# Kernel optimization log

Hardware: AMD Instinct MI355X
Metric: run time of the kernel (lower is better)

The kernel has to match this reference:

```python
import jax, jax.numpy as jnp
import numpy as np

B, N, NC, T, C, H = 8, 16, 16, 64, 512, 8


def setup_inputs() -> dict:
    key = jax.random.key(0)
    ks = jax.random.split(key, 7)
    s = 1.0 / np.sqrt(C)  # ~kaiming-uniform scale for Linear weights
    x = jax.random.normal(ks[0], (B, N, T, C), dtype=jnp.float32)
    c = jax.random.normal(ks[1], (B, NC, T, C), dtype=jnp.float32)
    mask = jax.random.randint(ks[2], (B, N * T, (N + NC) * T), 0, 2).astype(bool)
    Wq = jax.random.normal(ks[3], (C, C), dtype=jnp.float32) * s  # [out, in], torch Linear layout
    Wk = jax.random.normal(ks[4], (C, C), dtype=jnp.float32) * s
    Wv = jax.random.normal(ks[5], (C, C), dtype=jnp.float32) * s
    Wp = jax.random.normal(ks[6], (C, C), dtype=jnp.float32) * s
    return {"x": x, "c": c, "mask": mask, "Wq": Wq, "Wk": Wk, "Wv": Wv, "Wp": Wp}


def reference(x, c, mask, Wq, Wk, Wv, Wp):
    Bx, Nx, Tx, Cx = x.shape
    Dh = Cx // H
    kv_in = jnp.concatenate([x, c], axis=1)           # hybrid: [B, N+NC, T, C]
    Nk = kv_in.shape[1]
    # torch Linear: y = x @ W.T  -> einsum '...c,dc->...d'
    q = jnp.einsum('bntc,dc->bntd', x, Wq).reshape(Bx, Nx * Tx, H, Dh).transpose(0, 2, 1, 3)
    k = jnp.einsum('bntc,dc->bntd', kv_in, Wk).reshape(Bx, Nk * Tx, H, Dh).transpose(0, 2, 1, 3)
    v = jnp.einsum('bntc,dc->bntd', kv_in, Wv).reshape(Bx, Nk * Tx, H, Dh).transpose(0, 2, 1, 3)
    att = jnp.einsum('bhqd,bhkd->bhqk', q, k) * (1.0 / np.sqrt(Dh))  # [B,H,NT,NkT]
    att = jnp.where(mask[:, None, :, :], -jnp.inf, att)
    att = jax.nn.softmax(att, axis=-1)
    y = jnp.einsum('bhqk,bhkd->bhqd', att, v)          # [B,H,NT,Dh]
    y = y.transpose(0, 2, 1, 3).reshape(Bx, Nx * Tx, Cx)
    y = jnp.einsum('btc,dc->btd', y, Wp)
    return y.reshape(Bx, Nx, Tx, Cx)
```

## Files before the change

kernel.cpp:

```cpp
#include <hip/hip_runtime.h>
#include <hip/hip_bf16.h>
#include <stdint.h>

typedef __bf16 v8bf __attribute__((ext_vector_type(8)));
typedef short v4s __attribute__((ext_vector_type(4)));
typedef float f32x4 __attribute__((ext_vector_type(4)));

__device__ __forceinline__ void gload_lds16(const void* g, void* l) {
    __builtin_amdgcn_global_load_lds(
        (const __attribute__((address_space(1))) void*)g,
        (__attribute__((address_space(3))) void*)l, 16, 0, 0);
}

__device__ __forceinline__ unsigned short f2bf(float f) {
    __hip_bfloat16 h = __float2bfloat16(f);
    return __builtin_bit_cast(unsigned short, h);
}

__device__ __forceinline__ f32x4 mfma16x16x16bf(v4s a, v4s b, f32x4 c) {
#if __has_builtin(__builtin_amdgcn_mfma_f32_16x16x16bf16_1k)
    return __builtin_amdgcn_mfma_f32_16x16x16bf16_1k(a, b, c, 0, 0, 0);
#elif __has_builtin(__builtin_amdgcn_mfma_f32_16x16x16_bf16)
    return __builtin_amdgcn_mfma_f32_16x16x16_bf16(a, b, c, 0, 0, 0);
#else
    asm("s_nop 1\n\t"
        "v_mfma_f32_16x16x16_bf16 %0, %1, %2, %0\n\t"
        "s_nop 7\n\ts_nop 3"
        : "+v"(c) : "v"(a), "v"(b));
    return c;
#endif
}

__global__ __launch_bounds__(256) void cvt_xcw(const float* __restrict__ x,
                                               const float* __restrict__ c,
                                               const float* __restrict__ wq,
                                               const float* __restrict__ wk,
                                               const float* __restrict__ wv,
                                               const float* __restrict__ wp,
                                               __hip_bfloat16* __restrict__ xc,
                                               __hip_bfloat16* __restrict__ wout) {
    int bid = blockIdx.x;
    if (bid < 8192) {
        int i = bid * 256 + threadIdx.x;
        long e = (long)i * 4;
        int b = (int)(e >> 20);
        int rem = (int)(e & ((1 << 20) - 1));
        int r = rem >> 9;
        int col = rem & 511;
        const float* src = (r < 1024) ? (x + ((long)b << 19) + (long)r * 512 + col)
                                      : (c + ((long)b << 19) + (long)(r - 1024) * 512 + col);
        float4 v = *(const float4*)src;
        ushort4 o;
        o.x = f2bf(v.x); o.y = f2bf(v.y); o.z = f2bf(v.z); o.w = f2bf(v.w);
        ((ushort4*)xc)[i] = o;
    } else {
        int i = (bid - 8192) * 256 + threadIdx.x;
        int e = i * 4;
        int w = e >> 18;
        int off = e & ((1 << 18) - 1);
        const float* src = (w == 0 ? wq : w == 1 ? wk : w == 2 ? wv : wp) + off;
        float4 val = *(const float4*)src;
        ushort4 o;
        o.x = f2bf(val.x); o.y = f2bf(val.y); o.z = f2bf(val.z); o.w = f2bf(val.w);
        ((ushort4*)wout)[i] = o;
    }
}

__global__ __launch_bounds__(256) void cvt_mask(const int* __restrict__ mask,
                                                unsigned long long* __restrict__ mbt) {
    int t = threadIdx.x;
    long base = (long)blockIdx.x * 1024;
#pragma unroll
    for (int j = 0; j < 4; j++) {
        long i = base + j * 256 + t;
        int v = mask[i] != 0;
        unsigned long long bits = __ballot(v);
        if ((t & 63) == 0) {
            int b = (int)(i >> 21);
            int q = (int)((i >> 11) & 1023);
            int word = (int)((i >> 6) & 31);
            mbt[((long)b * 32 + word) * 1024 + q] = bits;
        }
    }
}

__global__ __launch_bounds__(256) void gemm_qkv(const __hip_bfloat16* __restrict__ A,
                                                const __hip_bfloat16* __restrict__ Bw,
                                                __hip_bfloat16* __restrict__ Qw,
                                                __hip_bfloat16* __restrict__ Kw,
                                                __hip_bfloat16* __restrict__ Vtw) {
    __shared__ union {
        struct { __hip_bfloat16 As[128 * 32]; __hip_bfloat16 Bs[128 * 32]; } s;
        __hip_bfloat16 T[128 * 136];
    } u;
    const int tid = threadIdx.x;
    const int wave = tid >> 6, lane = tid & 63;
    const int m0 = blockIdx.x * 128, n0 = blockIdx.y * 128;

    const int la = lane >> 2;
    const int kc = (lane & 3) * 8;
    const long ga0 = (long)(m0 + wave * 16 + la) * 512 + kc;
    const long ga1 = (long)(m0 + (wave + 4) * 16 + la) * 512 + kc;
    const long gb0 = (long)(n0 + wave * 16 + la) * 512 + kc;
    const long gb1 = (long)(n0 + (wave + 4) * 16 + la) * 512 + kc;

    f32x4 acc[4][4] = {};
    const int mw = (wave & 1) * 64, nw = (wave >> 1) * 64;
    const int lrow = lane & 15, lk = (lane >> 4) * 8;

    for (int k0 = 0; k0 < 512; k0 += 32) {
        gload_lds16(A + ga0 + k0, &u.s.As[wave * 512]);
        gload_lds16(A + ga1 + k0, &u.s.As[(wave + 4) * 512]);
        gload_lds16(Bw + gb0 + k0, &u.s.Bs[wave * 512]);
        gload_lds16(Bw + gb1 + k0, &u.s.Bs[(wave + 4) * 512]);
        __syncthreads();
        v8bf a[4], b[4];
#pragma unroll
        for (int i = 0; i < 4; i++) {
            a[i] = *(const v8bf*)&u.s.As[(mw + i * 16 + lrow) * 32 + lk];
            b[i] = *(const v8bf*)&u.s.Bs[(nw + i * 16 + lrow) * 32 + lk];
        }
#pragma unroll
        for (int mi = 0; mi < 4; mi++)
#pragma unroll
            for (int ni = 0; ni < 4; ni++)
                acc[mi][ni] = __builtin_amdgcn_mfma_f32_16x16x32_bf16(a[mi], b[ni], acc[mi][ni], 0, 0, 0);
        __syncthreads();
    }

    const int lq = lane >> 4;
    if (blockIdx.y < 8) {
#pragma unroll
        for (int mi = 0; mi < 4; mi++)
#pragma unroll
            for (int ni = 0; ni < 4; ni++)
#pragma unroll
                for (int r = 0; r < 4; r++) {
                    int grow = m0 + mw + mi * 16 + lq * 4 + r;
                    int gcol = n0 + nw + ni * 16 + lrow;
                    int w = gcol >> 9, g9 = gcol & 511;
                    int h = g9 >> 6, dh = g9 & 63;
                    int b_ = grow >> 11, rr = grow & 2047;
                    float val = acc[mi][ni][r];
                    if (w == 0) {
                        if (rr < 1024)
                            Qw[((long)(b_ * 8 + h) * 1024 + rr) * 64 + dh] =
                                __float2bfloat16(val * 0.1803368801f);
                    } else {
                        Kw[((long)(b_ * 8 + h) * 2048 + rr) * 64 + dh] = __float2bfloat16(val);
                    }
                }
    } else {
#pragma unroll
        for (int mi = 0; mi < 4; mi++)
#pragma unroll
            for (int ni = 0; ni < 4; ni++) {
                int n_l = nw + ni * 16 + lrow;
                int m_l = mw + mi * 16 + lq * 4;
                ushort4 pk;
                pk.x = f2bf(acc[mi][ni][0]); pk.y = f2bf(acc[mi][ni][1]);
                pk.z = f2bf(acc[mi][ni][2]); pk.w = f2bf(acc[mi][ni][3]);
                *(ushort4*)&u.T[n_l * 136 + m_l] = pk;
            }
        __syncthreads();
        const int no = (blockIdx.y - 8) * 128;
        const int b_ = m0 >> 11, rrb = m0 & 2047;
#pragma unroll
        for (int i = 0; i < 8; i++) {
            int s = tid + i * 256;
            int n_l = s >> 4, ch = s & 15;
            int ng = no + n_l;
            int h = ng >> 6, dh = ng & 63;
            uint4 v = *(const uint4*)&u.T[n_l * 136 + ch * 8];
            *(uint4*)&Vtw[((long)(b_ * 8 + h) * 64 + dh) * 2048 + rrb + ch * 8] = v;
        }
    }
}

__global__ __launch_bounds__(256) void gemm_out(const __hip_bfloat16* __restrict__ A,
                                                const __hip_bfloat16* __restrict__ Bw,
                                                float* __restrict__ outp) {
    __shared__ __hip_bfloat16 As[128 * 32];
    __shared__ __hip_bfloat16 Bs[128 * 32];
    const int tid = threadIdx.x;
    const int wave = tid >> 6, lane = tid & 63;
    const int m0 = blockIdx.x * 128, n0 = blockIdx.y * 128;

    const int la = lane >> 2;
    const int kc = (lane & 3) * 8;
    const long ga0 = (long)(m0 + wave * 16 + la) * 512 + kc;
    const long ga1 = (long)(m0 + (wave + 4) * 16 + la) * 512 + kc;
    const long gb0 = (long)(n0 + wave * 16 + la) * 512 + kc;
    const long gb1 = (long)(n0 + (wave + 4) * 16 + la) * 512 + kc;

    f32x4 acc[4][4] = {};
    const int mw = (wave & 1) * 64, nw = (wave >> 1) * 64;
    const int lrow = lane & 15, lk = (lane >> 4) * 8;

    for (int k0 = 0; k0 < 512; k0 += 32) {
        gload_lds16(A + ga0 + k0, &As[wave * 512]);
        gload_lds16(A + ga1 + k0, &As[(wave + 4) * 512]);
        gload_lds16(Bw + gb0 + k0, &Bs[wave * 512]);
        gload_lds16(Bw + gb1 + k0, &Bs[(wave + 4) * 512]);
        __syncthreads();
        v8bf a[4], b[4];
#pragma unroll
        for (int i = 0; i < 4; i++) {
            a[i] = *(const v8bf*)&As[(mw + i * 16 + lrow) * 32 + lk];
            b[i] = *(const v8bf*)&Bs[(nw + i * 16 + lrow) * 32 + lk];
        }
#pragma unroll
        for (int mi = 0; mi < 4; mi++)
#pragma unroll
            for (int ni = 0; ni < 4; ni++)
                acc[mi][ni] = __builtin_amdgcn_mfma_f32_16x16x32_bf16(a[mi], b[ni], acc[mi][ni], 0, 0, 0);
        __syncthreads();
    }

    const int lq = lane >> 4;
#pragma unroll
    for (int mi = 0; mi < 4; mi++)
#pragma unroll
        for (int ni = 0; ni < 4; ni++)
#pragma unroll
            for (int r = 0; r < 4; r++) {
                int grow = m0 + mw + mi * 16 + lq * 4 + r;
                int gcol = n0 + nw + ni * 16 + lrow;
                outp[(long)grow * 512 + gcol] = acc[mi][ni][r];
            }
}

__global__ __launch_bounds__(256) void flash(const __hip_bfloat16* __restrict__ Q,
                                             const __hip_bfloat16* __restrict__ K,
                                             const __hip_bfloat16* __restrict__ Vt,
                                             const unsigned long long* __restrict__ Mbt,
                                             __hip_bfloat16* __restrict__ Y) {
    constexpr int LDT = 72;
    __shared__ __hip_bfloat16 Ks[2][64 * LDT];
    __shared__ __hip_bfloat16 Vts[2][64 * LDT];

    const int L = blockIdx.x;
    const int b = L & 7, qt = (L >> 3) & 15, h = L >> 7;
    const int bh = b * 8 + h;
    const int tid = threadIdx.x, w = tid >> 6, lane = tid & 63;
    const int lcol = lane & 15, lq = lane >> 4;

    const __hip_bfloat16* Qp = Q + ((long)bh * 1024 + qt * 64 + w * 16 + lcol) * 64 + lq * 8;
    const __hip_bfloat16* Kg = K + (long)bh * 2048 * 64;
    const __hip_bfloat16* Vg = Vt + (long)bh * 64 * 2048;
    const unsigned long long* Mp = Mbt + (long)b * 32 * 1024 + qt * 64 + w * 16 + lcol;

    const int u0 = tid, u1 = tid + 256;
    const int r0 = u0 >> 3, p0 = u0 & 7;
    const int r1 = u1 >> 3, p1 = u1 & 7;

    v8bf bq0 = *(const v8bf*)(Qp);
    v8bf bq1 = *(const v8bf*)(Qp + 32);

    f32x4 O[4] = {};
    float lsum = 0.f;

    {
        const uint4* ksrc = (const uint4*)Kg;
        uint4 k0 = ksrc[u0], k1 = ksrc[u1];
        uint4 v0 = *(const uint4*)(Vg + (long)r0 * 2048 + p0 * 8);
        uint4 v1 = *(const uint4*)(Vg + (long)r1 * 2048 + p1 * 8);
        *(uint4*)&Ks[0][r0 * LDT + p0 * 8] = k0;
        *(uint4*)&Ks[0][r1 * LDT + p1 * 8] = k1;
        *(uint4*)&Vts[0][r0 * LDT + p0 * 8] = v0;
        *(uint4*)&Vts[0][r1 * LDT + p1 * 8] = v1;
    }
    __syncthreads();

    int cur = 0;
    for (int kt = 0; kt < 32; kt++) {
        unsigned long long mword = Mp[(long)kt * 1024];

        uint4 nk0, nk1, nv0, nv1;
        if (kt < 31) {
            const uint4* ksrc = (const uint4*)(Kg + ((kt + 1) << 12));
            nk0 = ksrc[u0];
            nk1 = ksrc[u1];
            nv0 = *(const uint4*)(Vg + (long)r0 * 2048 + (kt + 1) * 64 + p0 * 8);
            nv1 = *(const uint4*)(Vg + (long)r1 * 2048 + (kt + 1) * 64 + p1 * 8);
        }

        const __hip_bfloat16* Kb = Ks[cur];
        const __hip_bfloat16* Vb = Vts[cur];
#pragma unroll
        for (int nt = 0; nt < 4; nt++) {
            v8bf ak0 = *(const v8bf*)&Kb[(nt * 16 + lcol) * LDT + lq * 8];
            v8bf ak1 = *(const v8bf*)&Kb[(nt * 16 + lcol) * LDT + 32 + lq * 8];
            f32x4 st = {};
            __builtin_amdgcn_s_setprio(1);
            st = __builtin_amdgcn_mfma_f32_16x16x32_bf16(ak0, bq0, st, 0, 0, 0);
            st = __builtin_amdgcn_mfma_f32_16x16x32_bf16(ak1, bq1, st, 0, 0, 0);
            __builtin_amdgcn_s_setprio(0);
            unsigned int nib = (unsigned int)(mword >> (nt * 16 + lq * 4)) & 0xFu;
            float e0 = ((nib >> 0) & 1u) ? 0.f : __builtin_amdgcn_exp2f(fminf(st[0], 57.f));
            float e1 = ((nib >> 1) & 1u) ? 0.f : __builtin_amdgcn_exp2f(fminf(st[1], 57.f));
            float e2 = ((nib >> 2) & 1u) ? 0.f : __builtin_amdgcn_exp2f(fminf(st[2], 57.f));
            float e3 = ((nib >> 3) & 1u) ? 0.f : __builtin_amdgcn_exp2f(fminf(st[3], 57.f));
            lsum += (e0 + e1) + (e2 + e3);
            __hip_bfloat162 lo = __float22bfloat162_rn(make_float2(e0, e1));
            __hip_bfloat162 hi = __float22bfloat162_rn(make_float2(e2, e3));
            uint2 pku;
            __builtin_memcpy(&pku.x, &lo, 4);
            __builtin_memcpy(&pku.y, &hi, 4);
            v4s pa = __builtin_bit_cast(v4s, pku);
            __builtin_amdgcn_s_setprio(1);
#pragma unroll
            for (int nd = 0; nd < 4; nd++) {
                v4s bv = *(const v4s*)&Vb[(nd * 16 + lcol) * LDT + nt * 16 + lq * 4];
                O[nd] = mfma16x16x16bf(pa, bv, O[nd]);
            }
            __builtin_amdgcn_s_setprio(0);
        }

        if (kt < 31) {
            __hip_bfloat16* Kw_ = Ks[cur ^ 1];
            __hip_bfloat16* Vw_ = Vts[cur ^ 1];
            *(uint4*)&Kw_[r0 * LDT + p0 * 8] = nk0;
            *(uint4*)&Kw_[r1 * LDT + p1 * 8] = nk1;
            *(uint4*)&Vw_[r0 * LDT + p0 * 8] = nv0;
            *(uint4*)&Vw_[r1 * LDT + p1 * 8] = nv1;
        }
        __syncthreads();
        cur ^= 1;
    }

    float s = lsum;
    s += __shfl_xor(s, 16);
    s += __shfl_xor(s, 32);
    float inv[4];
#pragma unroll
    for (int r = 0; r < 4; r++) inv[r] = 1.f / __shfl(s, lq * 4 + r);

    __hip_bfloat16* Yp = Y + ((long)b * 1024 + qt * 64 + w * 16) * 512 + h * 64 + lcol;
#pragma unroll
    for (int nd = 0; nd < 4; nd++)
#pragma unroll
        for (int r = 0; r < 4; r++)
            Yp[(long)(lq * 4 + r) * 512 + nd * 16] = __float2bfloat16(O[nd][r] * inv[r]);
}

extern "C" void kernel_launch(void* const* d_in, const int* in_sizes, int n_in,
                              void* d_out, int out_size, void* d_ws, size_t ws_size,
                              hipStream_t stream) {
    const float* x = (const float*)d_in[0];
    const float* c = (const float*)d_in[1];
    const int* mask = (const int*)d_in[2];
    const float* Wq = (const float*)d_in[3];
    const float* Wk = (const float*)d_in[4];
    const float* Wv = (const float*)d_in[5];
    const float* Wp = (const float*)d_in[6];

    char* ws = (char*)d_ws;
    __hip_bfloat16* xc  = (__hip_bfloat16*)(ws);
    __hip_bfloat16* Wbf = (__hip_bfloat16*)(ws + 16777216);
    __hip_bfloat16* Qw  = (__hip_bfloat16*)(ws + 18874368);
    __hip_bfloat16* Kw  = (__hip_bfloat16*)(ws + 27262976);
    __hip_bfloat16* Vtw = (__hip_bfloat16*)(ws + 44040192);
    __hip_bfloat16* Yb  = (__hip_bfloat16*)(ws + 60817408);
    unsigned long long* Mbp = (unsigned long long*)(ws);

    cvt_xcw<<<9216, 256, 0, stream>>>(x, c, Wq, Wk, Wv, Wp, xc, Wbf);
    gemm_qkv<<<dim3(128, 12), 256, 0, stream>>>(xc, Wbf, Qw, Kw, Vtw);
    cvt_mask<<<16384, 256, 0, stream>>>(mask, Mbp);
    flash<<<1024, 256, 0, stream>>>(Qw, Kw, Vtw, Mbp, Yb);
    gemm_out<<<dim3(64, 4), 256, 0, stream>>>(Yb, Wbf + 3 * 262144, (float*)d_out);
}
```

Baseline: 281.0 us.

## Double-buffer LDS tiles in QKV/out GEMMs and prefetch mask word in flash

```diff
diff --git a/kernel.cpp b/kernel.cpp
--- a/kernel.cpp
+++ b/kernel.cpp
@@ -90,8 +90,8 @@
                                                 __hip_bfloat16* __restrict__ Kw,
                                                 __hip_bfloat16* __restrict__ Vtw) {
     __shared__ union {
-        struct { __hip_bfloat16 As[128 * 32]; __hip_bfloat16 Bs[128 * 32]; } s;
-        __hip_bfloat16 T[128 * 136];
+        struct { __hip_bfloat16 As[2][128 * 32]; __hip_bfloat16 Bs[2][128 * 32]; } s;
+        __hip_bfloat16 T[64 * 136];
     } u;
     const int tid = threadIdx.x;
     const int wave = tid >> 6, lane = tid & 63;
@@ -108,23 +108,34 @@
     const int mw = (wave & 1) * 64, nw = (wave >> 1) * 64;
     const int lrow = lane & 15, lk = (lane >> 4) * 8;
 
-    for (int k0 = 0; k0 < 512; k0 += 32) {
-        gload_lds16(A + ga0 + k0, &u.s.As[wave * 512]);
-        gload_lds16(A + ga1 + k0, &u.s.As[(wave + 4) * 512]);
-        gload_lds16(Bw + gb0 + k0, &u.s.Bs[wave * 512]);
-        gload_lds16(Bw + gb1 + k0, &u.s.Bs[(wave + 4) * 512]);
-        __syncthreads();
+    gload_lds16(A + ga0, &u.s.As[0][wave * 512]);
+    gload_lds16(A + ga1, &u.s.As[0][(wave + 4) * 512]);
+    gload_lds16(Bw + gb0, &u.s.Bs[0][wave * 512]);
+    gload_lds16(Bw + gb1, &u.s.Bs[0][(wave + 4) * 512]);
+    __syncthreads();
+
+    for (int it = 0; it < 16; ++it) {
+        const int cur = it & 1;
+        if (it < 15) {
+            const int k0 = (it + 1) * 32;
+            gload_lds16(A + ga0 + k0, &u.s.As[cur ^ 1][wave * 512]);
+            gload_lds16(A + ga1 + k0, &u.s.As[cur ^ 1][(wave + 4) * 512]);
+            gload_lds16(Bw + gb0 + k0, &u.s.Bs[cur ^ 1][wave * 512]);
+            gload_lds16(Bw + gb1 + k0, &u.s.Bs[cur ^ 1][(wave + 4) * 512]);
+        }
         v8bf a[4], b[4];
 #pragma unroll
         for (int i = 0; i < 4; i++) {
-            a[i] = *(const v8bf*)&u.s.As[(mw + i * 16 + lrow) * 32 + lk];
-            b[i] = *(const v8bf*)&u.s.Bs[(nw + i * 16 + lrow) * 32 + lk];
-        }
+            a[i] = *(const v8bf*)&u.s.As[cur][(mw + i * 16 + lrow) * 32 + lk];
+            b[i] = *(const v8bf*)&u.s.Bs[cur][(nw + i * 16 + lrow) * 32 + lk];
+        }
+        __builtin_amdgcn_s_setprio(1);
 #pragma unroll
         for (int mi = 0; mi < 4; mi++)
 #pragma unroll
             for (int ni = 0; ni < 4; ni++)
                 acc[mi][ni] = __builtin_amdgcn_mfma_f32_16x16x32_bf16(a[mi], b[ni], acc[mi][ni], 0, 0, 0);
+        __builtin_amdgcn_s_setprio(0);
         __syncthreads();
     }
 
@@ -151,28 +162,34 @@
                     }
                 }
     } else {
-#pragma unroll
-        for (int mi = 0; mi < 4; mi++)
-#pragma unroll
-            for (int ni = 0; ni < 4; ni++) {
-                int n_l = nw + ni * 16 + lrow;
-                int m_l = mw + mi * 16 + lq * 4;
-                ushort4 pk;
-                pk.x = f2bf(acc[mi][ni][0]); pk.y = f2bf(acc[mi][ni][1]);
-                pk.z = f2bf(acc[mi][ni][2]); pk.w = f2bf(acc[mi][ni][3]);
-                *(ushort4*)&u.T[n_l * 136 + m_l] = pk;
-            }
-        __syncthreads();
         const int no = (blockIdx.y - 8) * 128;
         const int b_ = m0 >> 11, rrb = m0 & 2047;
 #pragma unroll
-        for (int i = 0; i < 8; i++) {
-            int s = tid + i * 256;
-            int n_l = s >> 4, ch = s & 15;
-            int ng = no + n_l;
-            int h = ng >> 6, dh = ng & 63;
-            uint4 v = *(const uint4*)&u.T[n_l * 136 + ch * 8];
-            *(uint4*)&Vtw[((long)(b_ * 8 + h) * 64 + dh) * 2048 + rrb + ch * 8] = v;
+        for (int pass = 0; pass < 2; ++pass) {
+            __syncthreads();
+            if ((wave >> 1) == pass) {
+#pragma unroll
+                for (int mi = 0; mi < 4; mi++)
+#pragma unroll
+                    for (int ni = 0; ni < 4; ni++) {
+                        int n_l = ni * 16 + lrow;
+                        int m_l = mw + mi * 16 + lq * 4;
+                        ushort4 pk;
+                        pk.x = f2bf(acc[mi][ni][0]); pk.y = f2bf(acc[mi][ni][1]);
+                        pk.z = f2bf(acc[mi][ni][2]); pk.w = f2bf(acc[mi][ni][3]);
+                        *(ushort4*)&u.T[n_l * 136 + m_l] = pk;
+                    }
+            }
+            __syncthreads();
+#pragma unroll
+            for (int i = 0; i < 4; i++) {
+                int sI = tid + i * 256;
+                int n_l = sI >> 4, ch = sI & 15;
+                int ng = no + pass * 64 + n_l;
+                int h = ng >> 6, dh = ng & 63;
+                uint4 v = *(const uint4*)&u.T[n_l * 136 + ch * 8];
+                *(uint4*)&Vtw[((long)(b_ * 8 + h) * 64 + dh) * 2048 + rrb + ch * 8] = v;
+            }
         }
     }
 }
@@ -180,8 +197,8 @@
 __global__ __launch_bounds__(256) void gemm_out(const __hip_bfloat16* __restrict__ A,
                                                 const __hip_bfloat16* __restrict__ Bw,
                                                 float* __restrict__ outp) {
-    __shared__ __hip_bfloat16 As[128 * 32];
-    __shared__ __hip_bfloat16 Bs[128 * 32];
+    __shared__ __hip_bfloat16 As[2][128 * 32];
+    __shared__ __hip_bfloat16 Bs[2][128 * 32];
     const int tid = threadIdx.x;
     const int wave = tid >> 6, lane = tid & 63;
     const int m0 = blockIdx.x * 128, n0 = blockIdx.y * 128;
@@ -197,23 +214,34 @@
     const int mw = (wave & 1) * 64, nw = (wave >> 1) * 64;
     const int lrow = lane & 15, lk = (lane >> 4) * 8;
 
-    for (int k0 = 0; k0 < 512; k0 += 32) {
-        gload_lds16(A + ga0 + k0, &As[wave * 512]);
-        gload_lds16(A + ga1 + k0, &As[(wave + 4) * 512]);
-        gload_lds16(Bw + gb0 + k0, &Bs[wave * 512]);
-        gload_lds16(Bw + gb1 + k0, &Bs[(wave + 4) * 512]);
-        __syncthreads();
+    gload_lds16(A + ga0, &As[0][wave * 512]);
+    gload_lds16(A + ga1, &As[0][(wave + 4) * 512]);
+    gload_lds16(Bw + gb0, &Bs[0][wave * 512]);
+    gload_lds16(Bw + gb1, &Bs[0][(wave + 4) * 512]);
+    __syncthreads();
+
+    for (int it = 0; it < 16; ++it) {
+        const int cur = it & 1;
+        if (it < 15) {
+            const int k0 = (it + 1) * 32;
+            gload_lds16(A + ga0 + k0, &As[cur ^ 1][wave * 512]);
+            gload_lds16(A + ga1 + k0, &As[cur ^ 1][(wave + 4) * 512]);
+            gload_lds16(Bw + gb0 + k0, &Bs[cur ^ 1][wave * 512]);
+            gload_lds16(Bw + gb1 + k0, &Bs[cur ^ 1][(wave + 4) * 512]);
+        }
         v8bf a[4], b[4];
 #pragma unroll
         for (int i = 0; i < 4; i++) {
-            a[i] = *(const v8bf*)&As[(mw + i * 16 + lrow) * 32 + lk];
-            b[i] = *(const v8bf*)&Bs[(nw + i * 16 + lrow) * 32 + lk];
-        }
+            a[i] = *(const v8bf*)&As[cur][(mw + i * 16 + lrow) * 32 + lk];
+            b[i] = *(const v8bf*)&Bs[cur][(nw + i * 16 + lrow) * 32 + lk];
+        }
+        __builtin_amdgcn_s_setprio(1);
 #pragma unroll
         for (int mi = 0; mi < 4; mi++)
 #pragma unroll
             for (int ni = 0; ni < 4; ni++)
                 acc[mi][ni] = __builtin_amdgcn_mfma_f32_16x16x32_bf16(a[mi], b[ni], acc[mi][ni], 0, 0, 0);
+        __builtin_amdgcn_s_setprio(0);
         __syncthreads();
     }
 
@@ -260,6 +288,7 @@
     f32x4 O[4] = {};
     float lsum = 0.f;
 
+    unsigned long long mword = Mp[0];
     {
         const uint4* ksrc = (const uint4*)Kg;
         uint4 k0 = ksrc[u0], k1 = ksrc[u1];
@@ -274,7 +303,7 @@
 
     int cur = 0;
     for (int kt = 0; kt < 32; kt++) {
-        unsigned long long mword = Mp[(long)kt * 1024];
+        const unsigned long long mcur = mword;
 
         uint4 nk0, nk1, nv0, nv1;
         if (kt < 31) {
@@ -283,6 +312,7 @@
             nk1 = ksrc[u1];
             nv0 = *(const uint4*)(Vg + (long)r0 * 2048 + (kt + 1) * 64 + p0 * 8);
             nv1 = *(const uint4*)(Vg + (long)r1 * 2048 + (kt + 1) * 64 + p1 * 8);
+            mword = Mp[(long)(kt + 1) * 1024];
         }
 
         const __hip_bfloat16* Kb = Ks[cur];
@@ -296,7 +326,7 @@
             st = __builtin_amdgcn_mfma_f32_16x16x32_bf16(ak0, bq0, st, 0, 0, 0);
             st = __builtin_amdgcn_mfma_f32_16x16x32_bf16(ak1, bq1, st, 0, 0, 0);
             __builtin_amdgcn_s_setprio(0);
-            unsigned int nib = (unsigned int)(mword >> (nt * 16 + lq * 4)) & 0xFu;
+            unsigned int nib = (unsigned int)(mcur >> (nt * 16 + lq * 4)) & 0xFu;
             float e0 = ((nib >> 0) & 1u) ? 0.f : __builtin_amdgcn_exp2f(fminf(st[0], 57.f));
             float e1 = ((nib >> 1) & 1u) ? 0.f : __builtin_amdgcn_exp2f(fminf(st[1], 57.f));
             float e2 = ((nib >> 2) & 1u) ? 0.f : __builtin_amdgcn_exp2f(fminf(st[2], 57.f));
```

New measurement: 276.7 us. Within noise of the previous version (-1.5%).
